# Kernel optimization log

Hardware: AMD Instinct MI355X
Metric: run time of the kernel (lower is better)

## Reference

```python
import jax, jax.numpy as jnp
import numpy as np

H = 192      # hidden size
B = 8        # number of trees (perfect binary trees)
L = 32       # leaves per tree (must be power of 2)
VOC = 32000  # vocabulary size
OUT = 5      # output classes (SST-5)


def setup_inputs() -> dict:
    key = jax.random.key(0)
    ks = jax.random.split(key, 6)
    s = 1.0 / np.sqrt(2 * H)
    return {
        "embed": jax.random.normal(ks[0], (VOC, H), jnp.float32) * 0.02,
        "Vt": jax.random.normal(ks[1], (H, 2 * H, 2 * H), jnp.float32) * s,  # stacked V list
        "W": jax.random.normal(ks[2], (2 * H, H), jnp.float32) * s,
        "b": jnp.zeros((1, H), jnp.float32),
        "Wout_w": jax.random.normal(ks[3], (OUT, H), jnp.float32) * 0.05,
        "Wout_b": jnp.zeros((OUT,), jnp.float32),
        "leaf_ids": jax.random.randint(ks[4], (B, L), 0, VOC),
    }


def reference(embed, Vt, W, b, Wout_w, Wout_b, leaf_ids):
    # Leaves: embedding lookup. [B, L, H]
    cur = embed[leaf_ids]
    nodes = [cur.reshape(-1, H)]
    # Process tree levels bottom-up; adjacent pairs are (left, right) siblings.
    while cur.shape[1] > 1:
        n = cur.shape[1]
        # concat([left, right], feature dim): [B, n//2, 2H]
        c = cur.reshape(cur.shape[0], n // 2, 2 * H)
        # bilinear slice products: x^T V_h x for each h -> [B, n//2, H]
        xVx = jnp.einsum('bnx,hxy,bny->bnh', c, Vt, c)
        Wx = jnp.einsum('bnx,xh->bnh', c, W)
        cur = jnp.tanh(xVx + Wx + b)  # b broadcasts [1, H]
        nodes.append(cur.reshape(-1, H))
    allv = jnp.concatenate(nodes, axis=0)  # [B*(2L-1), H]
    logits = allv @ Wout_w.T + Wout_b
    return jax.nn.log_softmax(logits, axis=-1)
```

## Files before the change

kernel.cpp:

```cpp
#include <hip/hip_runtime.h>
#include <hip/hip_bf16.h>

#define HD 192
#define H2 384
#define NB 8
#define NL 32
#define NOUT 5
#define MROWS 73728
#define VT_ELEMS 28311552

typedef __attribute__((ext_vector_type(4))) float f32x4;
typedef __attribute__((ext_vector_type(8))) short bf16x8;

__device__ __forceinline__ ushort f2bf(float f) {
    union { float f; unsigned u; } v; v.f = f;
    unsigned r = v.u + 0x7FFF + ((v.u >> 16) & 1);
    return (ushort)(r >> 16);
}
__device__ __forceinline__ float bf2f(ushort s) {
    union { unsigned u; float f; } v; v.u = ((unsigned)s) << 16;
    return v.f;
}

__global__ void convert_vt_kernel(const float* __restrict__ src, ushort* __restrict__ dst) {
    long long i = (long long)blockIdx.x * blockDim.x + threadIdx.x;
    long long stride = (long long)gridDim.x * blockDim.x;
    const long long n4 = VT_ELEMS / 4;
    for (long long j = i; j < n4; j += stride) {
        float4 v = ((const float4*)src)[j];
        ushort4 o; o.x = f2bf(v.x); o.y = f2bf(v.y); o.z = f2bf(v.z); o.w = f2bf(v.w);
        ((ushort4*)dst)[j] = o;
    }
}

__global__ void leaf_kernel(const float* __restrict__ embed, const int* __restrict__ leaf_ids,
                            float* __restrict__ nodes, ushort* __restrict__ C1,
                            ushort* __restrict__ C5) {
    int r = blockIdx.x;
    int t = threadIdx.x;
    int id = leaf_ids[r];
    float v = embed[(long long)id * HD + t];
    nodes[r * HD + t] = v;
    C1[r * HD + t] = f2bf(v);
    if (r == 0) {
        for (int i = t; i < 8 * H2; i += HD) C5[8 * H2 + i] = 0;
    }
}

template<int NT>
__global__ __launch_bounds__(256) void gemm1_kernel(const ushort* __restrict__ A,
                                                    const ushort* __restrict__ C,
                                                    ushort* __restrict__ D) {
    constexpr int NP = NT * 16;
    __shared__ ushort Clds[NP * 200];
    const int tid = threadIdx.x;
    const int lane = tid & 63, wave = tid >> 6;
    const int m0 = blockIdx.x * 128 + wave * 32;
    const int lr = lane & 15;
    const int lk = (lane >> 4) * 8;

    f32x4 acc[2][NT];
#pragma unroll
    for (int mi = 0; mi < 2; mi++)
#pragma unroll
        for (int ni = 0; ni < NT; ni++) acc[mi][ni] = (f32x4){0.f, 0.f, 0.f, 0.f};

#pragma unroll
    for (int kh = 0; kh < 2; kh++) {
        __syncthreads();
        for (int i = tid; i < NP * 24; i += 256) {
            int row = i / 24, c8 = (i % 24) * 8;
            *(uint4*)&Clds[row * 200 + c8] = *(const uint4*)&C[row * H2 + kh * 192 + c8];
        }
        __syncthreads();
#pragma unroll
        for (int kk = 0; kk < 6; kk++) {
            const int k0 = kk * 32;
            const int kg = kh * 192 + k0;
            bf16x8 a[2], b[NT];
#pragma unroll
            for (int mi = 0; mi < 2; mi++)
                a[mi] = *(const bf16x8*)&A[(long long)(m0 + mi * 16 + lr) * H2 + kg + lk];
#pragma unroll
            for (int ni = 0; ni < NT; ni++)
                b[ni] = *(const bf16x8*)&Clds[(ni * 16 + lr) * 200 + k0 + lk];
#pragma unroll
            for (int mi = 0; mi < 2; mi++)
#pragma unroll
                for (int ni = 0; ni < NT; ni++)
                    acc[mi][ni] = __builtin_amdgcn_mfma_f32_16x16x32_bf16(a[mi], b[ni], acc[mi][ni], 0, 0, 0);
        }
    }
    const int dr = (lane >> 4) * 4;
#pragma unroll
    for (int mi = 0; mi < 2; mi++)
#pragma unroll
        for (int ni = 0; ni < NT; ni++)
#pragma unroll
            for (int i = 0; i < 4; i++) {
                int row = m0 + mi * 16 + dr + i;
                int col = ni * 16 + lr;
                D[(long long)row * NP + col] = f2bf(acc[mi][ni][i]);
            }
}

__global__ __launch_bounds__(256) void reduce2_kernel(const ushort* __restrict__ D,
        const ushort* __restrict__ C, const float* __restrict__ W, const float* __restrict__ bb,
        float* __restrict__ outn, ushort* __restrict__ Cnext, int N, int log2N, int NP) {
    const int h = blockIdx.x, tid = threadIdx.x;
    __shared__ float wl[H2];
    __shared__ float red0[256], red1[256];
    for (int x = tid; x < H2; x += 256) wl[x] = W[x * HD + h];
    __syncthreads();
    const int n = tid & (N - 1);
    const int xs = tid >> log2N;
    const int XS = 256 >> log2N;
    float a1 = 0.f, a2 = 0.f;
#pragma unroll 4
    for (int x = xs; x < H2; x += XS) {
        float c = bf2f(C[n * H2 + x]);
        a1 += bf2f(D[(h * H2 + x) * NP + n]) * c;
        a2 += c * wl[x];
    }
    red0[tid] = a1; red1[tid] = a2;
    __syncthreads();
    for (int s = 128; s >= N; s >>= 1) {
        if (tid < s) { red0[tid] += red0[tid + s]; red1[tid] += red1[tid + s]; }
        __syncthreads();
    }
    if (tid < N) {
        float pre = red0[tid] + red1[tid] + bb[h];
        float t = tanhf(pre);
        outn[tid * HD + h] = t;
        if (Cnext) Cnext[tid * HD + h] = f2bf(t);
    }
}

__global__ void logits_kernel(const float* __restrict__ nodes, const float* __restrict__ Ww,
                              const float* __restrict__ Wb, float* __restrict__ out) {
    int r = blockIdx.x, t = threadIdx.x;
    __shared__ float lg[NOUT];
    if (t < NOUT) {
        float s = Wb[t];
        const float* a = nodes + r * HD;
        const float* w = Ww + t * HD;
#pragma unroll 8
        for (int k = 0; k < HD; k++) s += a[k] * w[k];
        lg[t] = s;
    }
    __syncthreads();
    if (t < NOUT) {
        float m = lg[0];
        for (int i = 1; i < NOUT; i++) m = fmaxf(m, lg[i]);
        float sum = 0.f;
        for (int i = 0; i < NOUT; i++) sum += expf(lg[i] - m);
        out[r * NOUT + t] = lg[t] - m - logf(sum);
    }
}

extern "C" void kernel_launch(void* const* d_in, const int* in_sizes, int n_in,
                              void* d_out, int out_size, void* d_ws, size_t ws_size,
                              hipStream_t stream) {
    const float* embed   = (const float*)d_in[0];
    const float* Vt      = (const float*)d_in[1];
    const float* W       = (const float*)d_in[2];
    const float* bb      = (const float*)d_in[3];
    const float* Ww      = (const float*)d_in[4];
    const float* Wb      = (const float*)d_in[5];
    const int*   leaf_ids= (const int*)d_in[6];
    float* out = (float*)d_out;

    char* ws = (char*)d_ws;
    size_t off = 0;
    ushort* Vtb  = (ushort*)(ws + off); off += (size_t)VT_ELEMS * 2;
    float*  nodes= (float*) (ws + off); off += (size_t)504 * HD * 4;
    ushort* C1   = (ushort*)(ws + off); off += (size_t)128 * H2 * 2;
    ushort* C2   = (ushort*)(ws + off); off += (size_t)64  * H2 * 2;
    ushort* C3   = (ushort*)(ws + off); off += (size_t)32  * H2 * 2;
    ushort* C4   = (ushort*)(ws + off); off += (size_t)16  * H2 * 2;
    ushort* C5   = (ushort*)(ws + off); off += (size_t)16  * H2 * 2;
    ushort* D1   = (ushort*)(ws + off); off += (size_t)MROWS * 128 * 2;

    convert_vt_kernel<<<2048, 256, 0, stream>>>(Vt, Vtb);
    leaf_kernel<<<256, HD, 0, stream>>>(embed, leaf_ids, nodes, C1, C5);

    gemm1_kernel<8><<<576, 256, 0, stream>>>(Vtb, C1, D1);
    reduce2_kernel<<<HD, 256, 0, stream>>>(D1, C1, W, bb, nodes + 256 * HD, C2, 128, 7, 128);
    gemm1_kernel<4><<<576, 256, 0, stream>>>(Vtb, C2, D1);
    reduce2_kernel<<<HD, 256, 0, stream>>>(D1, C2, W, bb, nodes + 384 * HD, C3, 64, 6, 64);
    gemm1_kernel<2><<<576, 256, 0, stream>>>(Vtb, C3, D1);
    reduce2_kernel<<<HD, 256, 0, stream>>>(D1, C3, W, bb, nodes + 448 * HD, C4, 32, 5, 32);
    gemm1_kernel<1><<<576, 256, 0, stream>>>(Vtb, C4, D1);
    reduce2_kernel<<<HD, 256, 0, stream>>>(D1, C4, W, bb, nodes + 480 * HD, C5, 16, 4, 16);
    gemm1_kernel<1><<<576, 256, 0, stream>>>(Vtb, C5, D1);
    reduce2_kernel<<<HD, 256, 0, stream>>>(D1, C5, W, bb, nodes + 496 * HD, (ushort*)nullptr, 8, 3, 16);

    logits_kernel<<<504, 64, 0, stream>>>(nodes, Ww, Wb, out);
}
```

Before: 348.5 us.

## Fuse Vt bf16 conversion into first GEMM and reduce xVx in-kernel via atomics

The standalone fp32-to-bf16 conversion of Vt is folded into the first level's GEMM, which reads fp32 Vt, converts it in registers, and writes the bf16 copy for later levels. Each GEMM block now contracts its accumulator tile with the child vectors in the epilogue and atomically adds per-(h,n) partial sums. This removes the large D intermediate write and re-read by the reduce kernel. The epilogue kernel only adds the W term, bias and tanh, and zeroes the ping-pong accumulation buffer for the next level. The cost is float atomics with nondeterministic summation order, and the first GEMM does heavier fp32 loads.

```diff
diff --git a/kernel.cpp b/kernel.cpp
--- a/kernel.cpp
+++ b/kernel.cpp
@@ -3,14 +3,11 @@
 
 #define HD 192
 #define H2 384
-#define NB 8
-#define NL 32
 #define NOUT 5
-#define MROWS 73728
-#define VT_ELEMS 28311552
 
 typedef __attribute__((ext_vector_type(4))) float f32x4;
 typedef __attribute__((ext_vector_type(8))) short bf16x8;
+typedef long long ll;
 
 __device__ __forceinline__ ushort f2bf(float f) {
     union { float f; unsigned u; } v; v.f = f;
@@ -22,42 +19,34 @@
     return v.f;
 }
 
-__global__ void convert_vt_kernel(const float* __restrict__ src, ushort* __restrict__ dst) {
-    long long i = (long long)blockIdx.x * blockDim.x + threadIdx.x;
-    long long stride = (long long)gridDim.x * blockDim.x;
-    const long long n4 = VT_ELEMS / 4;
-    for (long long j = i; j < n4; j += stride) {
-        float4 v = ((const float4*)src)[j];
-        ushort4 o; o.x = f2bf(v.x); o.y = f2bf(v.y); o.z = f2bf(v.z); o.w = f2bf(v.w);
-        ((ushort4*)dst)[j] = o;
-    }
-}
-
 __global__ void leaf_kernel(const float* __restrict__ embed, const int* __restrict__ leaf_ids,
                             float* __restrict__ nodes, ushort* __restrict__ C1,
-                            ushort* __restrict__ C5) {
+                            ushort* __restrict__ C5, float* __restrict__ xA) {
     int r = blockIdx.x;
     int t = threadIdx.x;
     int id = leaf_ids[r];
-    float v = embed[(long long)id * HD + t];
+    float v = embed[(ll)id * HD + t];
     nodes[r * HD + t] = v;
     C1[r * HD + t] = f2bf(v);
+    int idx = r * HD + t;
+    if (idx < HD * 128) xA[idx] = 0.f;
     if (r == 0) {
         for (int i = t; i < 8 * H2; i += HD) C5[8 * H2 + i] = 0;
     }
 }
 
-template<int NT>
-__global__ __launch_bounds__(256) void gemm1_kernel(const ushort* __restrict__ A,
-                                                    const ushort* __restrict__ C,
-                                                    ushort* __restrict__ D) {
+template<int NT, bool CVT>
+__global__ __launch_bounds__(256) void gemm_kernel(const void* __restrict__ Av,
+        const ushort* __restrict__ C, float* __restrict__ xVx, ushort* __restrict__ VtbOut) {
     constexpr int NP = NT * 16;
     __shared__ ushort Clds[NP * 200];
-    const int tid = threadIdx.x;
-    const int lane = tid & 63, wave = tid >> 6;
-    const int m0 = blockIdx.x * 128 + wave * 32;
-    const int lr = lane & 15;
-    const int lk = (lane >> 4) * 8;
+    __shared__ float red[4][NP];
+    const int tid = threadIdx.x, lane = tid & 63, wave = tid >> 6;
+    const int blk = blockIdx.x;
+    const int m0 = blk * 128 + wave * 32;
+    const int h  = blk / 3;
+    const int x0 = (blk % 3) * 128;
+    const int lr = lane & 15, dr = (lane >> 4) * 4, lk = (lane >> 4) * 8;
 
     f32x4 acc[2][NT];
 #pragma unroll
@@ -75,12 +64,26 @@
         __syncthreads();
 #pragma unroll
         for (int kk = 0; kk < 6; kk++) {
-            const int k0 = kk * 32;
-            const int kg = kh * 192 + k0;
+            const int k0 = kk * 32, kg = kh * 192 + k0;
             bf16x8 a[2], b[NT];
 #pragma unroll
-            for (int mi = 0; mi < 2; mi++)
-                a[mi] = *(const bf16x8*)&A[(long long)(m0 + mi * 16 + lr) * H2 + kg + lk];
+            for (int mi = 0; mi < 2; mi++) {
+                const ll rowoff = (ll)(m0 + mi * 16 + lr) * H2 + kg + lk;
+                if constexpr (CVT) {
+                    const float* ap = (const float*)Av + rowoff;
+                    float4 u0 = *(const float4*)ap;
+                    float4 u1 = *(const float4*)(ap + 4);
+                    bf16x8 f;
+                    f[0] = (short)f2bf(u0.x); f[1] = (short)f2bf(u0.y);
+                    f[2] = (short)f2bf(u0.z); f[3] = (short)f2bf(u0.w);
+                    f[4] = (short)f2bf(u1.x); f[5] = (short)f2bf(u1.y);
+                    f[6] = (short)f2bf(u1.z); f[7] = (short)f2bf(u1.w);
+                    a[mi] = f;
+                    *(bf16x8*)&VtbOut[rowoff] = f;
+                } else {
+                    a[mi] = *(const bf16x8*)&((const ushort*)Av)[rowoff];
+                }
+            }
 #pragma unroll
             for (int ni = 0; ni < NT; ni++)
                 b[ni] = *(const bf16x8*)&Clds[(ni * 16 + lr) * 200 + k0 + lk];
@@ -91,48 +94,59 @@
                     acc[mi][ni] = __builtin_amdgcn_mfma_f32_16x16x32_bf16(a[mi], b[ni], acc[mi][ni], 0, 0, 0);
         }
     }
-    const int dr = (lane >> 4) * 4;
-#pragma unroll
-    for (int mi = 0; mi < 2; mi++)
-#pragma unroll
-        for (int ni = 0; ni < NT; ni++)
-#pragma unroll
-            for (int i = 0; i < 4; i++) {
-                int row = m0 + mi * 16 + dr + i;
-                int col = ni * 16 + lr;
-                D[(long long)row * NP + col] = f2bf(acc[mi][ni][i]);
-            }
-}
-
-__global__ __launch_bounds__(256) void reduce2_kernel(const ushort* __restrict__ D,
+    float part[NT];
+#pragma unroll
+    for (int ni = 0; ni < NT; ni++) {
+        float p = 0.f;
+#pragma unroll
+        for (int mi = 0; mi < 2; mi++) {
+            int xb = x0 + wave * 32 + mi * 16 + dr;
+            ushort4 cv = *(const ushort4*)&C[(ni * 16 + lr) * H2 + xb];
+            p += acc[mi][ni][0] * bf2f(cv.x) + acc[mi][ni][1] * bf2f(cv.y)
+               + acc[mi][ni][2] * bf2f(cv.z) + acc[mi][ni][3] * bf2f(cv.w);
+        }
+        p += __shfl_xor(p, 16);
+        p += __shfl_xor(p, 32);
+        part[ni] = p;
+    }
+    if (lane < 16) {
+#pragma unroll
+        for (int ni = 0; ni < NT; ni++) red[wave][ni * 16 + lane] = part[ni];
+    }
+    __syncthreads();
+    if (tid < NP) {
+        float s = red[0][tid] + red[1][tid] + red[2][tid] + red[3][tid];
+        atomicAdd(&xVx[h * NP + tid], s);
+    }
+}
+
+__global__ __launch_bounds__(256) void epilogue_kernel(const float* __restrict__ xVx,
         const ushort* __restrict__ C, const float* __restrict__ W, const float* __restrict__ bb,
-        float* __restrict__ outn, ushort* __restrict__ Cnext, int N, int log2N, int NP) {
+        float* __restrict__ outn, ushort* __restrict__ Cnext,
+        float* __restrict__ zbuf, int zcount, int N, int log2N, int NP) {
     const int h = blockIdx.x, tid = threadIdx.x;
     __shared__ float wl[H2];
-    __shared__ float red0[256], red1[256];
+    __shared__ float red[256];
     for (int x = tid; x < H2; x += 256) wl[x] = W[x * HD + h];
     __syncthreads();
-    const int n = tid & (N - 1);
-    const int xs = tid >> log2N;
-    const int XS = 256 >> log2N;
-    float a1 = 0.f, a2 = 0.f;
-#pragma unroll 4
-    for (int x = xs; x < H2; x += XS) {
-        float c = bf2f(C[n * H2 + x]);
-        a1 += bf2f(D[(h * H2 + x) * NP + n]) * c;
-        a2 += c * wl[x];
-    }
-    red0[tid] = a1; red1[tid] = a2;
+    const int n = tid & (N - 1), xs = tid >> log2N, XS = 256 >> log2N;
+    float a = 0.f;
+    for (int x = xs; x < H2; x += XS) a += bf2f(C[n * H2 + x]) * wl[x];
+    red[tid] = a;
     __syncthreads();
     for (int s = 128; s >= N; s >>= 1) {
-        if (tid < s) { red0[tid] += red0[tid + s]; red1[tid] += red1[tid + s]; }
+        if (tid < s) red[tid] += red[tid + s];
         __syncthreads();
     }
     if (tid < N) {
-        float pre = red0[tid] + red1[tid] + bb[h];
+        float pre = xVx[h * NP + tid] + red[tid] + bb[h];
         float t = tanhf(pre);
         outn[tid * HD + h] = t;
         if (Cnext) Cnext[tid * HD + h] = f2bf(t);
+    }
+    if (zbuf) {
+        int idx = h * 256 + tid;
+        if (idx < zcount) zbuf[idx] = 0.f;
     }
 }
 
@@ -161,39 +175,40 @@
 extern "C" void kernel_launch(void* const* d_in, const int* in_sizes, int n_in,
                               void* d_out, int out_size, void* d_ws, size_t ws_size,
                               hipStream_t stream) {
-    const float* embed   = (const float*)d_in[0];
-    const float* Vt      = (const float*)d_in[1];
-    const float* W       = (const float*)d_in[2];
-    const float* bb      = (const float*)d_in[3];
-    const float* Ww      = (const float*)d_in[4];
-    const float* Wb      = (const float*)d_in[5];
-    const int*   leaf_ids= (const int*)d_in[6];
+    const float* embed    = (const float*)d_in[0];
+    const float* Vt       = (const float*)d_in[1];
+    const float* W        = (const float*)d_in[2];
+    const float* bb       = (const float*)d_in[3];
+    const float* Ww       = (const float*)d_in[4];
+    const float* Wb       = (const float*)d_in[5];
+    const int*   leaf_ids = (const int*)d_in[6];
     float* out = (float*)d_out;
 
     char* ws = (char*)d_ws;
     size_t off = 0;
-    ushort* Vtb  = (ushort*)(ws + off); off += (size_t)VT_ELEMS * 2;
+    ushort* Vtb  = (ushort*)(ws + off); off += (size_t)73728 * H2 * 2;
     float*  nodes= (float*) (ws + off); off += (size_t)504 * HD * 4;
     ushort* C1   = (ushort*)(ws + off); off += (size_t)128 * H2 * 2;
     ushort* C2   = (ushort*)(ws + off); off += (size_t)64  * H2 * 2;
     ushort* C3   = (ushort*)(ws + off); off += (size_t)32  * H2 * 2;
     ushort* C4   = (ushort*)(ws + off); off += (size_t)16  * H2 * 2;
     ushort* C5   = (ushort*)(ws + off); off += (size_t)16  * H2 * 2;
-    ushort* D1   = (ushort*)(ws + off); off += (size_t)MROWS * 128 * 2;
-
-    convert_vt_kernel<<<2048, 256, 0, stream>>>(Vt, Vtb);
-    leaf_kernel<<<256, HD, 0, stream>>>(embed, leaf_ids, nodes, C1, C5);
-
-    gemm1_kernel<8><<<576, 256, 0, stream>>>(Vtb, C1, D1);
-    reduce2_kernel<<<HD, 256, 0, stream>>>(D1, C1, W, bb, nodes + 256 * HD, C2, 128, 7, 128);
-    gemm1_kernel<4><<<576, 256, 0, stream>>>(Vtb, C2, D1);
-    reduce2_kernel<<<HD, 256, 0, stream>>>(D1, C2, W, bb, nodes + 384 * HD, C3, 64, 6, 64);
-    gemm1_kernel<2><<<576, 256, 0, stream>>>(Vtb, C3, D1);
-    reduce2_kernel<<<HD, 256, 0, stream>>>(D1, C3, W, bb, nodes + 448 * HD, C4, 32, 5, 32);
-    gemm1_kernel<1><<<576, 256, 0, stream>>>(Vtb, C4, D1);
-    reduce2_kernel<<<HD, 256, 0, stream>>>(D1, C4, W, bb, nodes + 480 * HD, C5, 16, 4, 16);
-    gemm1_kernel<1><<<576, 256, 0, stream>>>(Vtb, C5, D1);
-    reduce2_kernel<<<HD, 256, 0, stream>>>(D1, C5, W, bb, nodes + 496 * HD, (ushort*)nullptr, 8, 3, 16);
+    float*  xA   = (float*) (ws + off); off += (size_t)HD * 128 * 4;
+    float*  xB   = (float*) (ws + off); off += (size_t)HD * 128 * 4;
+
+    leaf_kernel<<<256, HD, 0, stream>>>(embed, leaf_ids, nodes, C1, C5, xA);
+
+    gemm_kernel<8, true ><<<576, 256, 0, stream>>>(Vt,  C1, xA, Vtb);
+    epilogue_kernel<<<HD, 256, 0, stream>>>(xA, C1, W, bb, nodes + 256 * HD, C2, xB, HD * 64, 128, 7, 128);
+    gemm_kernel<4, false><<<576, 256, 0, stream>>>(Vtb, C2, xB, nullptr);
+    epilogue_kernel<<<HD, 256, 0, stream>>>(xB, C2, W, bb, nodes + 384 * HD, C3, xA, HD * 32, 64, 6, 64);
+    gemm_kernel<2, false><<<576, 256, 0, stream>>>(Vtb, C3, xA, nullptr);
+    epilogue_kernel<<<HD, 256, 0, stream>>>(xA, C3, W, bb, nodes + 448 * HD, C4, xB, HD * 16, 32, 5, 32);
+    gemm_kernel<1, false><<<576, 256, 0, stream>>>(Vtb, C4, xB, nullptr);
+    epilogue_kernel<<<HD, 256, 0, stream>>>(xB, C4, W, bb, nodes + 480 * HD, C5, xA, HD * 16, 16, 4, 16);
+    gemm_kernel<1, false><<<576, 256, 0, stream>>>(Vtb, C5, xA, nullptr);
+    epilogue_kernel<<<HD, 256, 0, stream>>>(xA, C5, W, bb, nodes + 496 * HD, (ushort*)nullptr,
+                                            (float*)nullptr, 0, 8, 3, 16);
 
     logits_kernel<<<504, 64, 0, stream>>>(nodes, Ww, Wb, out);
 }
```

After: 343.2 us. About the same (-1.5%).
